# Kernel optimization log

Measured on AMD Instinct MI355X. Metric: run time of the kernel, lower is better.

The kernel has to match this reference:

```python
import jax, jax.numpy as jnp
import numpy as np

N_NODES = 50000
N_EDGES = 800000
N_GRAPHS = 64
IN_DIM, HID, OUT = 128, 128, 16


def gcn_conv(x, src, dst, deg_inv_sqrt, W, b):
    # x: [N, Cin]; src/dst: [E+N] (self-loops appended); W: [Cin, Cout]
    h = x @ W                                   # [N, Cout]
    norm = deg_inv_sqrt[src] * deg_inv_sqrt[dst]  # [E+N]
    msg = h[src] * norm[:, None]                # gather + scale
    out = jax.ops.segment_sum(msg, dst, num_segments=N_NODES)
    return out + b


def setup_inputs() -> dict:
    key = jax.random.key(0)
    ks = jax.random.split(key, 8)
    x = jax.random.normal(ks[0], (N_NODES, IN_DIM), dtype=jnp.float32)
    edge_index = jax.random.randint(ks[1], (2, N_EDGES), 0, N_NODES, dtype=jnp.int64)
    batch = jnp.sort(jax.random.randint(ks[2], (N_NODES,), 0, N_GRAPHS, dtype=jnp.int64))
    s = 1.0 / np.sqrt(IN_DIM)
    W1 = jax.random.normal(ks[3], (IN_DIM, HID), dtype=jnp.float32) * s
    b1 = jnp.zeros((HID,), dtype=jnp.float32)
    W2 = jax.random.normal(ks[4], (HID, HID), dtype=jnp.float32) * (1.0 / np.sqrt(HID))
    b2 = jnp.zeros((HID,), dtype=jnp.float32)
    Wfc = jax.random.normal(ks[5], (HID, OUT), dtype=jnp.float32) * (1.0 / np.sqrt(HID))
    bfc = jnp.zeros((OUT,), dtype=jnp.float32)
    return {"x": x, "edge_index": edge_index, "batch": batch,
            "W1": W1, "b1": b1, "W2": W2, "b2": b2, "Wfc": Wfc, "bfc": bfc}


def reference(x, edge_index, batch, W1, b1, W2, b2, Wfc, bfc):
    self_loops = jnp.arange(N_NODES, dtype=edge_index.dtype)
    src = jnp.concatenate([edge_index[0], self_loops])  # [E+N]
    dst = jnp.concatenate([edge_index[1], self_loops])
    deg = jax.ops.segment_sum(jnp.ones_like(dst, dtype=x.dtype), dst, num_segments=N_NODES)
    deg_inv_sqrt = jnp.where(deg > 0, jax.lax.rsqrt(deg), 0.0)

    h = jax.nn.relu(gcn_conv(x, src, dst, deg_inv_sqrt, W1, b1))
    h = jax.nn.relu(gcn_conv(h, src, dst, deg_inv_sqrt, W2, b2))

    # global mean pool over graphs
    sums = jax.ops.segment_sum(h, batch, num_segments=N_GRAPHS)         # [G, HID]
    cnts = jax.ops.segment_sum(jnp.ones((N_NODES,), h.dtype), batch, num_segments=N_GRAPHS)
    pooled = sums / jnp.maximum(cnts, 1.0)[:, None]

    return pooled @ Wfc + bfc  # [G, OUT]
```

## Files before the change

### kernel.cpp

```cpp
#include <hip/hip_runtime.h>
#include <math.h>

#define N_NODES 50000
#define N_EDGES 800000
#define N_GRAPHS 64
#define DIM 128
#define OUTD 16
#define POOL_BLOCKS 1024

#define BSHIFT 8
#define BNODES 256
#define NBUCK ((N_NODES + BNODES - 1) / BNODES)
#define TILE 2048
#define RCAP 8192

typedef __attribute__((ext_vector_type(8))) short short8;
typedef __attribute__((ext_vector_type(4))) float f32x4;

static __device__ __forceinline__ unsigned short f2bf(float f) {
    unsigned u = __float_as_uint(f);
    u += 0x7fffu + ((u >> 16) & 1u);
    return (unsigned short)(u >> 16);
}
static __device__ __forceinline__ float bfl(unsigned u) {
    return __uint_as_float(u << 16);
}
static __device__ __forceinline__ float bfh(unsigned u) {
    return __uint_as_float(u & 0xffff0000u);
}
static __device__ __forceinline__ float b2f(unsigned short u) {
    return __uint_as_float((unsigned)u << 16);
}

__global__ __launch_bounds__(256) void k_cnt(const int* __restrict__ dstp,
                                             int* __restrict__ bucket_tot) {
    __shared__ int c[NBUCK];
    int tid = threadIdx.x;
    for (int i = tid; i < NBUCK; i += 256) c[i] = 0;
    __syncthreads();
    int tile0 = blockIdx.x * TILE;
#pragma unroll
    for (int j = 0; j < TILE / 256; ++j) {
        int e = tile0 + j * 256 + tid;
        if (e < N_EDGES) atomicAdd(&c[dstp[e] >> BSHIFT], 1);
    }
    __syncthreads();
    for (int i = tid; i < NBUCK; i += 256)
        if (c[i]) atomicAdd(&bucket_tot[i], c[i]);
}

__global__ __launch_bounds__(256) void k_scanB(const int* __restrict__ tot,
                                               int* __restrict__ base,
                                               int* __restrict__ cursor,
                                               float* __restrict__ pool,
                                               float* __restrict__ pcnt) {
    __shared__ int s[256];
    int tid = threadIdx.x;
    int v = (tid < NBUCK) ? tot[tid] : 0;
    s[tid] = v;
    __syncthreads();
    for (int off = 1; off < 256; off <<= 1) {
        int t = (tid >= off) ? s[tid - off] : 0;
        __syncthreads();
        s[tid] += t;
        __syncthreads();
    }
    if (tid < NBUCK) {
        int b = s[tid] - v;
        base[tid] = b;
        cursor[tid] = b;
    }
    if (tid == 0) base[NBUCK] = N_EDGES;
    for (int i = tid; i < N_GRAPHS * DIM; i += 256) pool[i] = 0.f;
    if (tid < N_GRAPHS) pcnt[tid] = 0.f;
}

__global__ __launch_bounds__(256) void k_binA(const int* __restrict__ src,
                                              const int* __restrict__ dstp,
                                              int* __restrict__ bucket_cursor,
                                              unsigned* __restrict__ bucket_arr) {
    __shared__ int cnt[NBUCK];
    __shared__ int base[NBUCK];
    int tile0 = blockIdx.x * TILE;
    for (int i = threadIdx.x; i < NBUCK; i += 256) cnt[i] = 0;
    __syncthreads();
#pragma unroll
    for (int j = 0; j < TILE / 256; ++j) {
        int e = tile0 + j * 256 + threadIdx.x;
        if (e < N_EDGES) atomicAdd(&cnt[dstp[e] >> BSHIFT], 1);
    }
    __syncthreads();
    for (int i = threadIdx.x; i < NBUCK; i += 256) {
        int c = cnt[i];
        base[i] = c ? atomicAdd(&bucket_cursor[i], c) : 0;
        cnt[i] = 0;
    }
    __syncthreads();
#pragma unroll
    for (int j = 0; j < TILE / 256; ++j) {
        int e = tile0 + j * 256 + threadIdx.x;
        if (e < N_EDGES) {
            int d = dstp[e];
            int b = d >> BSHIFT;
            int p = base[b] + atomicAdd(&cnt[b], 1);
            bucket_arr[p] = (unsigned)src[e] | ((unsigned)(d & 255) << 16);
        }
    }
}

__global__ __launch_bounds__(256) void k_binB(const unsigned* __restrict__ barr,
                                              const int* __restrict__ base,
                                              int* __restrict__ row_off,
                                              float* __restrict__ dis,
                                              unsigned short* __restrict__ csr) {
    __shared__ unsigned raw[RCAP];
    __shared__ unsigned short stage[RCAP];
    __shared__ int hist[BNODES];
    __shared__ int scn[BNODES];
    int tid = threadIdx.x;
    int b = blockIdx.x;
    int n0 = b << BSHIFT;
    int rbase = base[b];
    int len = base[b + 1] - rbase;

    hist[tid] = 0;
    __syncthreads();
    for (int i = tid; i < len; i += 256) {
        unsigned ed = barr[rbase + i];
        if (i < RCAP) raw[i] = ed;
        atomicAdd(&hist[ed >> 16], 1);
    }
    __syncthreads();
    int v = hist[tid];
    scn[tid] = v;
    __syncthreads();
    for (int off = 1; off < 256; off <<= 1) {
        int t = (tid >= off) ? scn[tid - off] : 0;
        __syncthreads();
        scn[tid] += t;
        __syncthreads();
    }
    int excl = scn[tid] - v;
    int n = n0 + tid;
    if (n < N_NODES) {
        row_off[n] = rbase + excl;
        dis[n] = rsqrtf((float)(v + 1));
    }
    if (b == NBUCK - 1 && tid == 0) row_off[N_NODES] = N_EDGES;
    hist[tid] = excl;
    __syncthreads();
    for (int i = tid; i < len; i += 256) {
        unsigned ed = (i < RCAP) ? raw[i] : barr[rbase + i];
        int p = atomicAdd(&hist[ed >> 16], 1);
        unsigned short sv = (unsigned short)(ed & 0xffffu);
        if (p < RCAP) stage[p] = sv;
        else csr[rbase + p] = sv;
    }
    __syncthreads();
    int lim = min(len, RCAP);
    for (int i = tid; i < lim; i += 256)
        csr[rbase + i] = stage[i];
}

template <int BF16IN>
__global__ __launch_bounds__(256) void k_gemm(const void* __restrict__ Av,
                                              const float* __restrict__ Wg,
                                              unsigned short* __restrict__ C,
                                              int nrows) {
    __shared__ unsigned smem[34816 / 4];
    unsigned* Wl = smem;
    {
        int t = threadIdx.x;
        int p = t & 63;
        int kp = p * 2;
        int n0 = (t >> 6) * 32;
        int kstep = kp >> 5;
        int quad = (kp >> 3) & 3;
        int jw = (kp & 7) >> 1;
        const float* r0 = Wg + (size_t)kp * DIM;
        const float* r1 = r0 + DIM;
        int rot = (p >> 2) & 7;
#pragma unroll
        for (int i4 = 0; i4 < 8; ++i4) {
            int nb = ((i4 + rot) & 7) * 4;
            int n = n0 + nb;
            float4 lo = *(const float4*)(r0 + n);
            float4 hi = *(const float4*)(r1 + n);
            const float* lp = &lo.x;
            const float* hp = &hi.x;
#pragma unroll
            for (int ii = 0; ii < 4; ++ii) {
                int nn = n + ii;
                int ct = nn >> 4;
                int l  = quad * 16 + (nn & 15);
                unsigned vlo = f2bf(lp[ii]);
                unsigned vhi = f2bf(hp[ii]);
                Wl[(((kstep * 8 + ct) * 64) + l) * 4 + jw] = vlo | (vhi << 16);
            }
        }
    }
    __syncthreads();

    int wid  = threadIdx.x >> 6;
    int lane = threadIdx.x & 63;
    int m    = lane & 15;
    int quad = lane >> 4;
    int row0 = blockIdx.x * 128 + wid * 32;
    if (row0 >= nrows) return;

    int rA = row0 + m;      if (rA >= nrows) rA = nrows - 1;
    int rB = row0 + 16 + m; if (rB >= nrows) rB = nrows - 1;

    short8 af0[4], af1[4];
    if (BF16IN) {
        const unsigned short* arowA = (const unsigned short*)Av + (size_t)rA * DIM + quad * 8;
        const unsigned short* arowB = (const unsigned short*)Av + (size_t)rB * DIM + quad * 8;
#pragma unroll
        for (int ks = 0; ks < 4; ++ks) {
            af0[ks] = *(const short8*)(arowA + ks * 32);
            af1[ks] = *(const short8*)(arowB + ks * 32);
        }
    } else {
        const float* arowA = (const float*)Av + (size_t)rA * DIM + quad * 8;
        const float* arowB = (const float*)Av + (size_t)rB * DIM + quad * 8;
#pragma unroll
        for (int ks = 0; ks < 4; ++ks) {
            float4 lo = *(const float4*)(arowA + ks * 32);
            float4 hi = *(const float4*)(arowA + ks * 32 + 4);
            short8 f;
            f[0] = (short)f2bf(lo.x); f[1] = (short)f2bf(lo.y);
            f[2] = (short)f2bf(lo.z); f[3] = (short)f2bf(lo.w);
            f[4] = (short)f2bf(hi.x); f[5] = (short)f2bf(hi.y);
            f[6] = (short)f2bf(hi.z); f[7] = (short)f2bf(hi.w);
            af0[ks] = f;
            lo = *(const float4*)(arowB + ks * 32);
            hi = *(const float4*)(arowB + ks * 32 + 4);
            f[0] = (short)f2bf(lo.x); f[1] = (short)f2bf(lo.y);
            f[2] = (short)f2bf(lo.z); f[3] = (short)f2bf(lo.w);
            f[4] = (short)f2bf(hi.x); f[5] = (short)f2bf(hi.y);
            f[6] = (short)f2bf(hi.z); f[7] = (short)f2bf(hi.w);
            af1[ks] = f;
        }
    }

    f32x4 acc0[8], acc1[8];
#pragma unroll
    for (int ct = 0; ct < 8; ++ct) {
        acc0[ct] = (f32x4){0.f, 0.f, 0.f, 0.f};
        acc1[ct] = (f32x4){0.f, 0.f, 0.f, 0.f};
    }

    const short8* Wf = (const short8*)Wl;
#pragma unroll
    for (int ks = 0; ks < 4; ++ks) {
#pragma unroll
        for (int ct = 0; ct < 8; ++ct) {
            short8 bfrag = Wf[(ks * 8 + ct) * 64 + lane];
            acc0[ct] = __builtin_amdgcn_mfma_f32_16x16x32_bf16(af0[ks], bfrag, acc0[ct], 0, 0, 0);
            acc1[ct] = __builtin_amdgcn_mfma_f32_16x16x32_bf16(af1[ks], bfrag, acc1[ct], 0, 0, 0);
        }
    }

    __syncthreads();
    unsigned short* cs = (unsigned short*)smem + wid * 4352;
#pragma unroll
    for (int ct = 0; ct < 8; ++ct) {
#pragma unroll
        for (int reg = 0; reg < 4; ++reg) {
            cs[(quad * 4 + reg) * 136 + ct * 16 + m]      = f2bf(acc0[ct][reg]);
            cs[(16 + quad * 4 + reg) * 136 + ct * 16 + m] = f2bf(acc1[ct][reg]);
        }
    }
    const unsigned char* cb = (const unsigned char*)smem + wid * 8704;
#pragma unroll
    for (int i = 0; i < 8; ++i) {
        int rg = i * 4 + quad;
        int r = row0 + rg;
        if (r < nrows) {
            uint4 vv = *(const uint4*)(cb + rg * 272 + m * 16);
            *((uint4*)(C + (size_t)r * DIM) + m) = vv;
        }
    }
}

__global__ __launch_bounds__(256) void k_agg(const uint4* __restrict__ Hb4,
                                             const int* __restrict__ row_off,
                                             const unsigned short* __restrict__ csr,
                                             const float* __restrict__ dis,
                                             const float* __restrict__ bias,
                                             uint4* __restrict__ out) {
    int lane = threadIdx.x & 15;
    int node = blockIdx.x * 16 + (threadIdx.x >> 4);
    if (node >= N_NODES) return;

    float dn = dis[node];
    float wself = dn * dn;
    uint4 hp = Hb4[(size_t)node * 16 + lane];
    float a0[8], a1[8], a2[8], a3[8];
    a0[0] = wself * bfl(hp.x); a0[1] = wself * bfh(hp.x);
    a0[2] = wself * bfl(hp.y); a0[3] = wself * bfh(hp.y);
    a0[4] = wself * bfl(hp.z); a0[5] = wself * bfh(hp.z);
    a0[6] = wself * bfl(hp.w); a0[7] = wself * bfh(hp.w);
#pragma unroll
    for (int j = 0; j < 8; ++j) { a1[j] = 0.f; a2[j] = 0.f; a3[j] = 0.f; }

    int e = row_off[node], e1 = row_off[node + 1];
    for (; e + 4 <= e1; e += 4) {
        int s0 = csr[e];     int s1 = csr[e + 1];
        int s2 = csr[e + 2]; int s3 = csr[e + 3];
        uint4 g0 = Hb4[(size_t)s0 * 16 + lane];
        uint4 g1 = Hb4[(size_t)s1 * 16 + lane];
        uint4 g2 = Hb4[(size_t)s2 * 16 + lane];
        uint4 g3 = Hb4[(size_t)s3 * 16 + lane];
        float w0 = dn * dis[s0], w1 = dn * dis[s1];
        float w2 = dn * dis[s2], w3 = dn * dis[s3];
        a0[0] = fmaf(w0, bfl(g0.x), a0[0]); a0[1] = fmaf(w0, bfh(g0.x), a0[1]);
        a0[2] = fmaf(w0, bfl(g0.y), a0[2]); a0[3] = fmaf(w0, bfh(g0.y), a0[3]);
        a0[4] = fmaf(w0, bfl(g0.z), a0[4]); a0[5] = fmaf(w0, bfh(g0.z), a0[5]);
        a0[6] = fmaf(w0, bfl(g0.w), a0[6]); a0[7] = fmaf(w0, bfh(g0.w), a0[7]);
        a1[0] = fmaf(w1, bfl(g1.x), a1[0]); a1[1] = fmaf(w1, bfh(g1.x), a1[1]);
        a1[2] = fmaf(w1, bfl(g1.y), a1[2]); a1[3] = fmaf(w1, bfh(g1.y), a1[3]);
        a1[4] = fmaf(w1, bfl(g1.z), a1[4]); a1[5] = fmaf(w1, bfh(g1.z), a1[5]);
        a1[6] = fmaf(w1, bfl(g1.w), a1[6]); a1[7] = fmaf(w1, bfh(g1.w), a1[7]);
        a2[0] = fmaf(w2, bfl(g2.x), a2[0]); a2[1] = fmaf(w2, bfh(g2.x), a2[1]);
        a2[2] = fmaf(w2, bfl(g2.y), a2[2]); a2[3] = fmaf(w2, bfh(g2.y), a2[3]);
        a2[4] = fmaf(w2, bfl(g2.z), a2[4]); a2[5] = fmaf(w2, bfh(g2.z), a2[5]);
        a2[6] = fmaf(w2, bfl(g2.w), a2[6]); a2[7] = fmaf(w2, bfh(g2.w), a2[7]);
        a3[0] = fmaf(w3, bfl(g3.x), a3[0]); a3[1] = fmaf(w3, bfh(g3.x), a3[1]);
        a3[2] = fmaf(w3, bfl(g3.y), a3[2]); a3[3] = fmaf(w3, bfh(g3.y), a3[3]);
        a3[4] = fmaf(w3, bfl(g3.z), a3[4]); a3[5] = fmaf(w3, bfh(g3.z), a3[5]);
        a3[6] = fmaf(w3, bfl(g3.w), a3[6]); a3[7] = fmaf(w3, bfh(g3.w), a3[7]);
    }
    for (; e < e1; ++e) {
        int s = csr[e];
        uint4 g = Hb4[(size_t)s * 16 + lane];
        float w = dn * dis[s];
        a0[0] = fmaf(w, bfl(g.x), a0[0]); a0[1] = fmaf(w, bfh(g.x), a0[1]);
        a0[2] = fmaf(w, bfl(g.y), a0[2]); a0[3] = fmaf(w, bfh(g.y), a0[3]);
        a0[4] = fmaf(w, bfl(g.z), a0[4]); a0[5] = fmaf(w, bfh(g.z), a0[5]);
        a0[6] = fmaf(w, bfl(g.w), a0[6]); a0[7] = fmaf(w, bfh(g.w), a0[7]);
    }

    float4 b0 = ((const float4*)bias)[lane * 2];
    float4 b1v = ((const float4*)bias)[lane * 2 + 1];
    float r[8];
    r[0] = fmaxf(a0[0] + a1[0] + a2[0] + a3[0] + b0.x, 0.f);
    r[1] = fmaxf(a0[1] + a1[1] + a2[1] + a3[1] + b0.y, 0.f);
    r[2] = fmaxf(a0[2] + a1[2] + a2[2] + a3[2] + b0.z, 0.f);
    r[3] = fmaxf(a0[3] + a1[3] + a2[3] + a3[3] + b0.w, 0.f);
    r[4] = fmaxf(a0[4] + a1[4] + a2[4] + a3[4] + b1v.x, 0.f);
    r[5] = fmaxf(a0[5] + a1[5] + a2[5] + a3[5] + b1v.y, 0.f);
    r[6] = fmaxf(a0[6] + a1[6] + a2[6] + a3[6] + b1v.z, 0.f);
    r[7] = fmaxf(a0[7] + a1[7] + a2[7] + a3[7] + b1v.w, 0.f);
    uint4 ov;
    ov.x = (unsigned)f2bf(r[0]) | ((unsigned)f2bf(r[1]) << 16);
    ov.y = (unsigned)f2bf(r[2]) | ((unsigned)f2bf(r[3]) << 16);
    ov.z = (unsigned)f2bf(r[4]) | ((unsigned)f2bf(r[5]) << 16);
    ov.w = (unsigned)f2bf(r[6]) | ((unsigned)f2bf(r[7]) << 16);
    out[(size_t)node * 16 + lane] = ov;
}

__global__ __launch_bounds__(128) void k_pool(const unsigned short* __restrict__ h,
                                              const int* __restrict__ batch,
                                              float* __restrict__ pool,
                                              float* __restrict__ pcnt) {
    int chunk = (N_NODES + POOL_BLOCKS - 1) / POOL_BLOCKS;
    int n0 = blockIdx.x * chunk;
    int n1 = min(n0 + chunk, N_NODES);
    if (n0 >= n1) return;
    int c = threadIdx.x;
    int curg = batch[n0];
    float acc = 0.f;
    int count = 0;
    int n = n0;
    for (; n + 4 <= n1; ) {
        int g0 = batch[n], g3 = batch[n + 3];
        if (g0 == curg && g3 == curg) {
            float v0 = b2f(h[(size_t)(n + 0) * DIM + c]);
            float v1 = b2f(h[(size_t)(n + 1) * DIM + c]);
            float v2 = b2f(h[(size_t)(n + 2) * DIM + c]);
            float v3 = b2f(h[(size_t)(n + 3) * DIM + c]);
            acc += (v0 + v1) + (v2 + v3);
            count += 4;
            n += 4;
        } else {
            int g = g0;
            if (g != curg) {
                atomicAdd(&pool[curg * DIM + c], acc);
                if (c == 0) atomicAdd(&pcnt[curg], (float)count);
                acc = 0.f; count = 0; curg = g;
            }
            acc += b2f(h[(size_t)n * DIM + c]);
            count++;
            n += 1;
        }
    }
    for (; n < n1; ++n) {
        int g = batch[n];
        if (g != curg) {
            atomicAdd(&pool[curg * DIM + c], acc);
            if (c == 0) atomicAdd(&pcnt[curg], (float)count);
            acc = 0.f; count = 0; curg = g;
        }
        acc += b2f(h[(size_t)n * DIM + c]);
        count++;
    }
    atomicAdd(&pool[curg * DIM + c], acc);
    if (c == 0) atomicAdd(&pcnt[curg], (float)count);
}

__global__ void k_fc(const float* __restrict__ pool, const float* __restrict__ pcnt,
                     const float* __restrict__ Wfc, const float* __restrict__ bfc,
                     float* __restrict__ out) {
    int id = blockIdx.x * blockDim.x + threadIdx.x;
    if (id >= N_GRAPHS * OUTD) return;
    int g = id >> 4, o = id & 15;
    float inv = 1.0f / fmaxf(pcnt[g], 1.0f);
    float acc = bfc[o];
    const float* p = pool + g * DIM;
    for (int c = 0; c < DIM; ++c)
        acc = fmaf(p[c] * inv, Wfc[c * OUTD + o], acc);
    out[id] = acc;
}


extern "C" void kernel_launch(void* const* d_in, const int* in_sizes, int n_in,
                              void* d_out, int out_size, void* d_ws, size_t ws_size,
                              hipStream_t stream) {
    const float* x    = (const float*)d_in[0];
    const int*   ei   = (const int*)d_in[1];
    const int*   batch= (const int*)d_in[2];
    const float* W1   = (const float*)d_in[3];
    const float* b1   = (const float*)d_in[4];
    const float* W2   = (const float*)d_in[5];
    const float* b2   = (const float*)d_in[6];
    const float* Wfc  = (const float*)d_in[7];
    const float* bfc  = (const float*)d_in[8];
    float* out = (float*)d_out;

    char* ws = (char*)d_ws;
    size_t off = 0;
    auto alloc = [&](size_t bytes) -> char* {
        char* p = ws + off;
        off = (off + bytes + 255) & ~(size_t)255;
        return p;
    };
    int*      btot     = (int*)     alloc((size_t)NBUCK * 4);
    int*      bbase    = (int*)     alloc((size_t)(NBUCK + 1) * 4);
    int*      bcursor  = (int*)     alloc((size_t)NBUCK * 4);
    int*      row_off  = (int*)     alloc((size_t)(N_NODES + 1) * 4);
    float*    dis      = (float*)   alloc((size_t)N_NODES * 4);
    unsigned short* csr= (unsigned short*)alloc((size_t)N_EDGES * 2);
    unsigned* barr     = (unsigned*)alloc((size_t)N_EDGES * 4);
    float*    pool     = (float*)   alloc((size_t)N_GRAPHS * DIM * 4);
    float*    pcnt     = (float*)   alloc((size_t)N_GRAPHS * 4);
    unsigned short* Hb = (unsigned short*)alloc((size_t)N_NODES * DIM * 2);
    unsigned short* Hb2= (unsigned short*)alloc((size_t)N_NODES * DIM * 2);

    const int* src = ei;
    const int* dst = ei + N_EDGES;

    hipMemsetAsync(btot, 0, (size_t)NBUCK * 4, stream);

    int bin_grid = (N_EDGES + TILE - 1) / TILE;
    k_cnt<<<bin_grid, 256, 0, stream>>>(dst, btot);
    k_scanB<<<1, 256, 0, stream>>>(btot, bbase, bcursor, pool, pcnt);
    k_binA<<<bin_grid, 256, 0, stream>>>(src, dst, bcursor, barr);
    k_binB<<<NBUCK, 256, 0, stream>>>(barr, bbase, row_off, dis, csr);

    int gemm_grid = (N_NODES + 127) / 128;
    int agg_grid  = (N_NODES + 15) / 16;
    k_gemm<0><<<gemm_grid, 256, 0, stream>>>(x, W1, Hb, N_NODES);
    k_agg<<<agg_grid, 256, 0, stream>>>((const uint4*)Hb, row_off, csr, dis, b1, (uint4*)Hb2);
    k_gemm<1><<<gemm_grid, 256, 0, stream>>>(Hb2, W2, Hb, N_NODES);
    k_agg<<<agg_grid, 256, 0, stream>>>((const uint4*)Hb, row_off, csr, dis, b2, (uint4*)Hb2);
    k_pool<<<POOL_BLOCKS, DIM, 0, stream>>>(Hb2, batch, pool, pcnt);
    k_fc<<<(N_GRAPHS * OUTD + 255) / 256, 256, 0, stream>>>(pool, pcnt, Wfc, bfc, out);
}
```

Baseline: 235.0 us.

## Use fixed-capacity bucket slots to drop count pass; make GEMM persistent

```diff
diff --git a/kernel.cpp b/kernel.cpp
--- a/kernel.cpp
+++ b/kernel.cpp
@@ -13,6 +13,7 @@
 #define NBUCK ((N_NODES + BNODES - 1) / BNODES)
 #define TILE 2048
 #define RCAP 8192
+#define BSLOT 4864
 
 typedef __attribute__((ext_vector_type(8))) short short8;
 typedef __attribute__((ext_vector_type(4))) float f32x4;
@@ -32,45 +33,11 @@
     return __uint_as_float((unsigned)u << 16);
 }
 
-__global__ __launch_bounds__(256) void k_cnt(const int* __restrict__ dstp,
-                                             int* __restrict__ bucket_tot) {
-    __shared__ int c[NBUCK];
+__global__ __launch_bounds__(256) void k_init(int* __restrict__ cursor,
+                                              float* __restrict__ pool,
+                                              float* __restrict__ pcnt) {
     int tid = threadIdx.x;
-    for (int i = tid; i < NBUCK; i += 256) c[i] = 0;
-    __syncthreads();
-    int tile0 = blockIdx.x * TILE;
-#pragma unroll
-    for (int j = 0; j < TILE / 256; ++j) {
-        int e = tile0 + j * 256 + tid;
-        if (e < N_EDGES) atomicAdd(&c[dstp[e] >> BSHIFT], 1);
-    }
-    __syncthreads();
-    for (int i = tid; i < NBUCK; i += 256)
-        if (c[i]) atomicAdd(&bucket_tot[i], c[i]);
-}
-
-__global__ __launch_bounds__(256) void k_scanB(const int* __restrict__ tot,
-                                               int* __restrict__ base,
-                                               int* __restrict__ cursor,
-                                               float* __restrict__ pool,
-                                               float* __restrict__ pcnt) {
-    __shared__ int s[256];
-    int tid = threadIdx.x;
-    int v = (tid < NBUCK) ? tot[tid] : 0;
-    s[tid] = v;
-    __syncthreads();
-    for (int off = 1; off < 256; off <<= 1) {
-        int t = (tid >= off) ? s[tid - off] : 0;
-        __syncthreads();
-        s[tid] += t;
-        __syncthreads();
-    }
-    if (tid < NBUCK) {
-        int b = s[tid] - v;
-        base[tid] = b;
-        cursor[tid] = b;
-    }
-    if (tid == 0) base[NBUCK] = N_EDGES;
+    if (tid < NBUCK) cursor[tid] = tid * BSLOT;
     for (int i = tid; i < N_GRAPHS * DIM; i += 256) pool[i] = 0.f;
     if (tid < N_GRAPHS) pcnt[tid] = 0.f;
 }
@@ -85,9 +52,13 @@
     for (int i = threadIdx.x; i < NBUCK; i += 256) cnt[i] = 0;
     __syncthreads();
 #pragma unroll
-    for (int j = 0; j < TILE / 256; ++j) {
-        int e = tile0 + j * 256 + threadIdx.x;
-        if (e < N_EDGES) atomicAdd(&cnt[dstp[e] >> BSHIFT], 1);
+    for (int j = 0; j < TILE / 512; ++j) {
+        int e = tile0 + j * 512 + threadIdx.x * 2;
+        if (e < N_EDGES) {
+            int2 d = *(const int2*)(dstp + e);
+            atomicAdd(&cnt[d.x >> BSHIFT], 1);
+            atomicAdd(&cnt[d.y >> BSHIFT], 1);
+        }
     }
     __syncthreads();
     for (int i = threadIdx.x; i < NBUCK; i += 256) {
@@ -97,15 +68,34 @@
     }
     __syncthreads();
 #pragma unroll
-    for (int j = 0; j < TILE / 256; ++j) {
-        int e = tile0 + j * 256 + threadIdx.x;
+    for (int j = 0; j < TILE / 512; ++j) {
+        int e = tile0 + j * 512 + threadIdx.x * 2;
         if (e < N_EDGES) {
-            int d = dstp[e];
-            int b = d >> BSHIFT;
-            int p = base[b] + atomicAdd(&cnt[b], 1);
-            bucket_arr[p] = (unsigned)src[e] | ((unsigned)(d & 255) << 16);
-        }
-    }
+            int2 s = *(const int2*)(src + e);
+            int2 d = *(const int2*)(dstp + e);
+            int b0 = d.x >> BSHIFT, b1 = d.y >> BSHIFT;
+            int p0 = base[b0] + atomicAdd(&cnt[b0], 1);
+            bucket_arr[p0] = (unsigned)s.x | ((unsigned)(d.x & 255) << 16);
+            int p1 = base[b1] + atomicAdd(&cnt[b1], 1);
+            bucket_arr[p1] = (unsigned)s.y | ((unsigned)(d.y & 255) << 16);
+        }
+    }
+}
+
+__global__ __launch_bounds__(256) void k_bases(const int* __restrict__ cursor,
+                                               int* __restrict__ base) {
+    __shared__ int s[256];
+    int tid = threadIdx.x;
+    int v = (tid < NBUCK) ? (cursor[tid] - tid * BSLOT) : 0;
+    s[tid] = v;
+    __syncthreads();
+    for (int off = 1; off < 256; off <<= 1) {
+        int t = (tid >= off) ? s[tid - off] : 0;
+        __syncthreads();
+        s[tid] += t;
+        __syncthreads();
+    }
+    if (tid <= NBUCK) base[tid] = s[tid] - v;
 }
 
 __global__ __launch_bounds__(256) void k_binB(const unsigned* __restrict__ barr,
@@ -122,11 +112,12 @@
     int n0 = b << BSHIFT;
     int rbase = base[b];
     int len = base[b + 1] - rbase;
+    const unsigned* bin = barr + (size_t)b * BSLOT;
 
     hist[tid] = 0;
     __syncthreads();
     for (int i = tid; i < len; i += 256) {
-        unsigned ed = barr[rbase + i];
+        unsigned ed = bin[i];
         if (i < RCAP) raw[i] = ed;
         atomicAdd(&hist[ed >> 16], 1);
     }
@@ -150,7 +141,7 @@
     hist[tid] = excl;
     __syncthreads();
     for (int i = tid; i < len; i += 256) {
-        unsigned ed = (i < RCAP) ? raw[i] : barr[rbase + i];
+        unsigned ed = (i < RCAP) ? raw[i] : bin[i];
         int p = atomicAdd(&hist[ed >> 16], 1);
         unsigned short sv = (unsigned short)(ed & 0xffffu);
         if (p < RCAP) stage[p] = sv;
@@ -167,8 +158,9 @@
                                               const float* __restrict__ Wg,
                                               unsigned short* __restrict__ C,
                                               int nrows) {
-    __shared__ unsigned smem[34816 / 4];
-    unsigned* Wl = smem;
+    __shared__ unsigned smemW[32768 / 4];
+    __shared__ unsigned smemC[34816 / 4];
+    unsigned* Wl = smemW;
     {
         int t = threadIdx.x;
         int p = t & 63;
@@ -205,80 +197,83 @@
     int lane = threadIdx.x & 63;
     int m    = lane & 15;
     int quad = lane >> 4;
-    int row0 = blockIdx.x * 128 + wid * 32;
-    if (row0 >= nrows) return;
-
-    int rA = row0 + m;      if (rA >= nrows) rA = nrows - 1;
-    int rB = row0 + 16 + m; if (rB >= nrows) rB = nrows - 1;
-
-    short8 af0[4], af1[4];
-    if (BF16IN) {
-        const unsigned short* arowA = (const unsigned short*)Av + (size_t)rA * DIM + quad * 8;
-        const unsigned short* arowB = (const unsigned short*)Av + (size_t)rB * DIM + quad * 8;
+    const short8* Wf = (const short8*)Wl;
+    unsigned short* cs = (unsigned short*)smemC + wid * 4352;
+    const unsigned char* cb = (const unsigned char*)smemC + wid * 8704;
+
+    int ntiles = (nrows + 127) / 128;
+    for (int tile = blockIdx.x; tile < ntiles; tile += gridDim.x) {
+        int row0 = tile * 128 + wid * 32;
+        if (row0 >= nrows) continue;
+
+        int rA = row0 + m;      if (rA >= nrows) rA = nrows - 1;
+        int rB = row0 + 16 + m; if (rB >= nrows) rB = nrows - 1;
+
+        short8 af0[4], af1[4];
+        if (BF16IN) {
+            const unsigned short* arowA = (const unsigned short*)Av + (size_t)rA * DIM + quad * 8;
+            const unsigned short* arowB = (const unsigned short*)Av + (size_t)rB * DIM + quad * 8;
+#pragma unroll
+            for (int ks = 0; ks < 4; ++ks) {
+                af0[ks] = *(const short8*)(arowA + ks * 32);
+                af1[ks] = *(const short8*)(arowB + ks * 32);
+            }
+        } else {
+            const float* arowA = (const float*)Av + (size_t)rA * DIM + quad * 8;
+            const float* arowB = (const float*)Av + (size_t)rB * DIM + quad * 8;
+#pragma unroll
+            for (int ks = 0; ks < 4; ++ks) {
+                float4 lo = *(const float4*)(arowA + ks * 32);
+                float4 hi = *(const float4*)(arowA + ks * 32 + 4);
+                short8 f;
+                f[0] = (short)f2bf(lo.x); f[1] = (short)f2bf(lo.y);
+                f[2] = (short)f2bf(lo.z); f[3] = (short)f2bf(lo.w);
+                f[4] = (short)f2bf(hi.x); f[5] = (short)f2bf(hi.y);
+                f[6] = (short)f2bf(hi.z); f[7] = (short)f2bf(hi.w);
+                af0[ks] = f;
+                lo = *(const float4*)(arowB + ks * 32);
+                hi = *(const float4*)(arowB + ks * 32 + 4);
+                f[0] = (short)f2bf(lo.x); f[1] = (short)f2bf(lo.y);
+                f[2] = (short)f2bf(lo.z); f[3] = (short)f2bf(lo.w);
+                f[4] = (short)f2bf(hi.x); f[5] = (short)f2bf(hi.y);
+                f[6] = (short)f2bf(hi.z); f[7] = (short)f2bf(hi.w);
+                af1[ks] = f;
+            }
+        }
+
+        f32x4 acc0[8], acc1[8];
+#pragma unroll
+        for (int ct = 0; ct < 8; ++ct) {
+            acc0[ct] = (f32x4){0.f, 0.f, 0.f, 0.f};
+            acc1[ct] = (f32x4){0.f, 0.f, 0.f, 0.f};
+        }
+
 #pragma unroll
         for (int ks = 0; ks < 4; ++ks) {
-            af0[ks] = *(const short8*)(arowA + ks * 32);
-            af1[ks] = *(const short8*)(arowB + ks * 32);
-        }
-    } else {
-        const float* arowA = (const float*)Av + (size_t)rA * DIM + quad * 8;
-        const float* arowB = (const float*)Av + (size_t)rB * DIM + quad * 8;
-#pragma unroll
-        for (int ks = 0; ks < 4; ++ks) {
-            float4 lo = *(const float4*)(arowA + ks * 32);
-            float4 hi = *(const float4*)(arowA + ks * 32 + 4);
-            short8 f;
-            f[0] = (short)f2bf(lo.x); f[1] = (short)f2bf(lo.y);
-            f[2] = (short)f2bf(lo.z); f[3] = (short)f2bf(lo.w);
-            f[4] = (short)f2bf(hi.x); f[5] = (short)f2bf(hi.y);
-            f[6] = (short)f2bf(hi.z); f[7] = (short)f2bf(hi.w);
-            af0[ks] = f;
-            lo = *(const float4*)(arowB + ks * 32);
-            hi = *(const float4*)(arowB + ks * 32 + 4);
-            f[0] = (short)f2bf(lo.x); f[1] = (short)f2bf(lo.y);
-            f[2] = (short)f2bf(lo.z); f[3] = (short)f2bf(lo.w);
-            f[4] = (short)f2bf(hi.x); f[5] = (short)f2bf(hi.y);
-            f[6] = (short)f2bf(hi.z); f[7] = (short)f2bf(hi.w);
-            af1[ks] = f;
-        }
-    }
-
-    f32x4 acc0[8], acc1[8];
-#pragma unroll
-    for (int ct = 0; ct < 8; ++ct) {
-        acc0[ct] = (f32x4){0.f, 0.f, 0.f, 0.f};
-        acc1[ct] = (f32x4){0.f, 0.f, 0.f, 0.f};
-    }
-
-    const short8* Wf = (const short8*)Wl;
-#pragma unroll
-    for (int ks = 0; ks < 4; ++ks) {
+#pragma unroll
+            for (int ct = 0; ct < 8; ++ct) {
+                short8 bfrag = Wf[(ks * 8 + ct) * 64 + lane];
+                acc0[ct] = __builtin_amdgcn_mfma_f32_16x16x32_bf16(af0[ks], bfrag, acc0[ct], 0, 0, 0);
+                acc1[ct] = __builtin_amdgcn_mfma_f32_16x16x32_bf16(af1[ks], bfrag, acc1[ct], 0, 0, 0);
+            }
+        }
+
 #pragma unroll
         for (int ct = 0; ct < 8; ++ct) {
-            short8 bfrag = Wf[(ks * 8 + ct) * 64 + lane];
-            acc0[ct] = __builtin_amdgcn_mfma_f32_16x16x32_bf16(af0[ks], bfrag, acc0[ct], 0, 0, 0);
-            acc1[ct] = __builtin_amdgcn_mfma_f32_16x16x32_bf16(af1[ks], bfrag, acc1[ct], 0, 0, 0);
-        }
-    }
-
-    __syncthreads();
-    unsigned short* cs = (unsigned short*)smem + wid * 4352;
-#pragma unroll
-    for (int ct = 0; ct < 8; ++ct) {
-#pragma unroll
-        for (int reg = 0; reg < 4; ++reg) {
-            cs[(quad * 4 + reg) * 136 + ct * 16 + m]      = f2bf(acc0[ct][reg]);
-            cs[(16 + quad * 4 + reg) * 136 + ct * 16 + m] = f2bf(acc1[ct][reg]);
-        }
-    }
-    const unsigned char* cb = (const unsigned char*)smem + wid * 8704;
-#pragma unroll
-    for (int i = 0; i < 8; ++i) {
-        int rg = i * 4 + quad;
-        int r = row0 + rg;
-        if (r < nrows) {
-            uint4 vv = *(const uint4*)(cb + rg * 272 + m * 16);
-            *((uint4*)(C + (size_t)r * DIM) + m) = vv;
+#pragma unroll
+            for (int reg = 0; reg < 4; ++reg) {
+                cs[(quad * 4 + reg) * 136 + ct * 16 + m]      = f2bf(acc0[ct][reg]);
+                cs[(16 + quad * 4 + reg) * 136 + ct * 16 + m] = f2bf(acc1[ct][reg]);
+            }
+        }
+#pragma unroll
+        for (int i = 0; i < 8; ++i) {
+            int rg = i * 4 + quad;
+            int r = row0 + rg;
+            if (r < nrows) {
+                uint4 vv = *(const uint4*)(cb + rg * 272 + m * 16);
+                *((uint4*)(C + (size_t)r * DIM) + m) = vv;
+            }
         }
     }
 }
@@ -445,13 +440,12 @@
         off = (off + bytes + 255) & ~(size_t)255;
         return p;
     };
-    int*      btot     = (int*)     alloc((size_t)NBUCK * 4);
     int*      bbase    = (int*)     alloc((size_t)(NBUCK + 1) * 4);
     int*      bcursor  = (int*)     alloc((size_t)NBUCK * 4);
     int*      row_off  = (int*)     alloc((size_t)(N_NODES + 1) * 4);
     float*    dis      = (float*)   alloc((size_t)N_NODES * 4);
     unsigned short* csr= (unsigned short*)alloc((size_t)N_EDGES * 2);
-    unsigned* barr     = (unsigned*)alloc((size_t)N_EDGES * 4);
+    unsigned* barr     = (unsigned*)alloc((size_t)NBUCK * BSLOT * 4);
     float*    pool     = (float*)   alloc((size_t)N_GRAPHS * DIM * 4);
     float*    pcnt     = (float*)   alloc((size_t)N_GRAPHS * 4);
     unsigned short* Hb = (unsigned short*)alloc((size_t)N_NODES * DIM * 2);
@@ -460,19 +454,16 @@
     const int* src = ei;
     const int* dst = ei + N_EDGES;
 
-    hipMemsetAsync(btot, 0, (size_t)NBUCK * 4, stream);
-
     int bin_grid = (N_EDGES + TILE - 1) / TILE;
-    k_cnt<<<bin_grid, 256, 0, stream>>>(dst, btot);
-    k_scanB<<<1, 256, 0, stream>>>(btot, bbase, bcursor, pool, pcnt);
+    k_init<<<1, 256, 0, stream>>>(bcursor, pool, pcnt);
     k_binA<<<bin_grid, 256, 0, stream>>>(src, dst, bcursor, barr);
+    k_bases<<<1, 256, 0, stream>>>(bcursor, bbase);
     k_binB<<<NBUCK, 256, 0, stream>>>(barr, bbase, row_off, dis, csr);
 
-    int gemm_grid = (N_NODES + 127) / 128;
-    int agg_grid  = (N_NODES + 15) / 16;
-    k_gemm<0><<<gemm_grid, 256, 0, stream>>>(x, W1, Hb, N_NODES);
+    int agg_grid = (N_NODES + 15) / 16;
+    k_gemm<0><<<256, 256, 0, stream>>>(x, W1, Hb, N_NODES);
     k_agg<<<agg_grid, 256, 0, stream>>>((const uint4*)Hb, row_off, csr, dis, b1, (uint4*)Hb2);
-    k_gemm<1><<<gemm_grid, 256, 0, stream>>>(Hb2, W2, Hb, N_NODES);
+    k_gemm<1><<<256, 256, 0, stream>>>(Hb2, W2, Hb, N_NODES);
     k_agg<<<agg_grid, 256, 0, stream>>>((const uint4*)Hb, row_off, csr, dis, b2, (uint4*)Hb2);
     k_pool<<<POOL_BLOCKS, DIM, 0, stream>>>(Hb2, batch, pool, pcnt);
     k_fc<<<(N_GRAPHS * OUTD + 255) / 256, 256, 0, stream>>>(pool, pcnt, Wfc, bfc, out);
```

Result: faster. 219.5 us (-6.6%).
